# Kernel tuning notes

Measured on AMD Instinct MI355X. Metric: run time of the kernel, lower is better.

## Reference

```python
import jax, jax.numpy as jnp
import numpy as np

B, N, D, K = 32, 1024, 768, 512

def setup_inputs() -> dict:
    key = jax.random.key(0)
    k1, k2 = jax.random.split(key)
    img_feat_map = jax.random.normal(k1, (B, N, D), dtype=jnp.float32)
    codebook = jax.random.normal(k2, (K, D), dtype=jnp.float32)
    return {"img_feat_map": img_feat_map, "codebook": codebook}

def reference(img_feat_map, codebook):
    # squared L2 distances between each token and each codebook vector
    x_sq = jnp.sum(img_feat_map ** 2, axis=2, keepdims=True)          # [B,N,1]
    c_sq = jnp.sum(codebook ** 2, axis=1)[None, None, :]              # [1,1,K]
    dot = jnp.einsum('bnd,kd->bnk', img_feat_map, codebook)           # [B,N,K]
    distances = x_sq + c_sq - 2.0 * dot                               # [B,N,K]
    soft_assignments = jax.nn.softmax(-distances, axis=2)             # [B,N,K]
    # aggregate tokens per codebook slot
    aggregated = jnp.einsum('bnk,bnd->bkd', soft_assignments, img_feat_map)  # [B,K,D]
    return aggregated
```

## Files before the change

### kernel.cpp

```cpp
#include <hip/hip_runtime.h>
#include <math.h>

#define BB 32
#define NN 1024
#define DD 768
#define KK 512
#define MM (BB * NN)

typedef _Float16 half8 __attribute__((ext_vector_type(8)));
typedef _Float16 half4 __attribute__((ext_vector_type(4)));
typedef float floatx4 __attribute__((ext_vector_type(4)));

__device__ __forceinline__ void load_lds16(const void* g, void* l) {
    __builtin_amdgcn_global_load_lds(
        (const __attribute__((address_space(1))) unsigned int*)g,
        (__attribute__((address_space(3))) unsigned int*)l, 16, 0, 0);
}

__global__ __launch_bounds__(256) void prep_codebook(const float* __restrict__ cb,
                                                     _Float16* __restrict__ Cbh,
                                                     float* __restrict__ csq) {
    int k = blockIdx.x;
    const float* row = cb + (size_t)k * DD;
    _Float16* orow = Cbh + (size_t)k * DD;
    float s = 0.f;
    for (int d = threadIdx.x; d < DD; d += 256) {
        float v = row[d];
        s += v * v;
        orow[d] = (_Float16)v;
    }
    #pragma unroll
    for (int off = 32; off > 0; off >>= 1) s += __shfl_down(s, off);
    __shared__ float sm[4];
    int lane = threadIdx.x & 63, wid = threadIdx.x >> 6;
    if (lane == 0) sm[wid] = s;
    __syncthreads();
    if (threadIdx.x == 0) csq[k] = sm[0] + sm[1] + sm[2] + sm[3];
}

__global__ __launch_bounds__(512, 4) void fused_logits_softmax(
    const float* __restrict__ X,
    const _Float16* __restrict__ Cbh,
    const float* __restrict__ csq,
    _Float16* __restrict__ St,
    _Float16* __restrict__ Xt)
{
    __shared__ _Float16 Cs[2][512][32];
    __shared__ _Float16 Xs[2][64][32];
    __shared__ float redbuf[8][64];
    __shared__ float gred[64];

    const int t = threadIdx.x;
    const int w = t >> 6;
    const int lane = t & 63;
    const int l15 = lane & 15;
    const int quad = lane >> 4;
    const int wk = w * 64;
    const int gm0 = blockIdx.x * 64;
    const int b = gm0 >> 10;
    const int n0 = gm0 & 1023;

    const int qs = (quad ^ ((l15 >> 1) & 3)) * 8;

    float cs[4];
    #pragma unroll
    for (int ki = 0; ki < 4; ki++) cs[ki] = csq[wk + ki * 16 + l15];

    floatx4 acc[4][4] = {};

    const int cr = t >> 2;
    const int cq = (t & 3) ^ ((t >> 3) & 3);
    const float* xsrc = X + (size_t)(gm0 + cr) * DD + cq * 8;

    const int tdr = t >> 4;
    const int tn4 = (t & 15) * 4;

    float4 xa, xb;
    if (t < 256) { xa = *(const float4*)xsrc; xb = *(const float4*)(xsrc + 4); }

    #pragma unroll
    for (int c = 0; c < 4; c++)
        load_lds16(Cbh + (size_t)(c * 128 + cr) * DD + cq * 8,
                   (_Float16*)Cs[0] + (c * 512 + t) * 8);
    if (t < 256) {
        half8 h;
        h[0] = (_Float16)xa.x; h[1] = (_Float16)xa.y; h[2] = (_Float16)xa.z; h[3] = (_Float16)xa.w;
        h[4] = (_Float16)xb.x; h[5] = (_Float16)xb.y; h[6] = (_Float16)xb.z; h[7] = (_Float16)xb.w;
        *(half8*)&Xs[0][cr][(t & 3) * 8] = h;
        xa = *(const float4*)(xsrc + 32);
        xb = *(const float4*)(xsrc + 36);
    }
    __syncthreads();

    int cur = 0;
    for (int it = 0; it < 24; ++it) {
        const int d0 = it * 32;
        if (it + 1 < 24) {
            const int d0n = d0 + 32;
            #pragma unroll
            for (int c = 0; c < 4; c++)
                load_lds16(Cbh + (size_t)(c * 128 + cr) * DD + d0n + cq * 8,
                           (_Float16*)Cs[cur ^ 1] + (c * 512 + t) * 8);
            if (t < 256) {
                half8 h;
                h[0] = (_Float16)xa.x; h[1] = (_Float16)xa.y; h[2] = (_Float16)xa.z; h[3] = (_Float16)xa.w;
                h[4] = (_Float16)xb.x; h[5] = (_Float16)xb.y; h[6] = (_Float16)xb.z; h[7] = (_Float16)xb.w;
                *(half8*)&Xs[cur ^ 1][cr][(t & 3) * 8] = h;
                if (it + 2 < 24) {
                    xa = *(const float4*)(xsrc + (it + 2) * 32);
                    xb = *(const float4*)(xsrc + (it + 2) * 32 + 4);
                }
            }
        }
        {
            half4 xo;
            #pragma unroll
            for (int j = 0; j < 4; j++) {
                int n = tn4 + j;
                xo[j] = *((const _Float16*)Xs[cur] + n * 32 +
                          (((tdr >> 3) ^ ((n >> 1) & 3)) << 3) + (tdr & 7));
            }
            *(half4*)&Xt[((size_t)b * DD + d0 + tdr) * NN + n0 + tn4] = xo;
        }
        half8 af[4], bf[4];
        #pragma unroll
        for (int mi = 0; mi < 4; mi++)
            af[mi] = *(half8*)((_Float16*)Xs[cur] + (mi * 16 + l15) * 32 + qs);
        #pragma unroll
        for (int ki = 0; ki < 4; ki++)
            bf[ki] = *(half8*)((_Float16*)Cs[cur] + (wk + ki * 16 + l15) * 32 + qs);
        #pragma unroll
        for (int mi = 0; mi < 4; mi++)
            #pragma unroll
            for (int ki = 0; ki < 4; ki++)
                acc[mi][ki] = __builtin_amdgcn_mfma_f32_16x16x32_f16(af[mi], bf[ki], acc[mi][ki], 0, 0, 0);
        if (it + 1 < 24) { __syncthreads(); cur ^= 1; }
    }

    float pmax[4][4];
    #pragma unroll
    for (int mi = 0; mi < 4; mi++)
        #pragma unroll
        for (int r = 0; r < 4; r++) {
            float m = -1e30f;
            #pragma unroll
            for (int ki = 0; ki < 4; ki++)
                m = fmaxf(m, 2.f * acc[mi][ki][r] - cs[ki]);
            pmax[mi][r] = m;
        }
    #pragma unroll
    for (int off = 1; off < 16; off <<= 1)
        #pragma unroll
        for (int mi = 0; mi < 4; mi++)
            #pragma unroll
            for (int r = 0; r < 4; r++)
                pmax[mi][r] = fmaxf(pmax[mi][r], __shfl_xor(pmax[mi][r], off));
    if (l15 == 0) {
        #pragma unroll
        for (int mi = 0; mi < 4; mi++)
            #pragma unroll
            for (int r = 0; r < 4; r++)
                redbuf[w][mi * 16 + quad * 4 + r] = pmax[mi][r];
    }
    __syncthreads();
    if (t < 64) {
        float g = redbuf[0][t];
        #pragma unroll
        for (int wv = 1; wv < 8; wv++) g = fmaxf(g, redbuf[wv][t]);
        gred[t] = g;
    }
    __syncthreads();
    float gmax[4][4];
    #pragma unroll
    for (int mi = 0; mi < 4; mi++)
        #pragma unroll
        for (int r = 0; r < 4; r++)
            gmax[mi][r] = gred[mi * 16 + quad * 4 + r];

    float psum[4][4] = {};
    #pragma unroll
    for (int mi = 0; mi < 4; mi++)
        #pragma unroll
        for (int ki = 0; ki < 4; ki++) {
            floatx4 e;
            #pragma unroll
            for (int r = 0; r < 4; r++) {
                e[r] = __expf(2.f * acc[mi][ki][r] - cs[ki] - gmax[mi][r]);
                psum[mi][r] += e[r];
            }
            acc[mi][ki] = e;
        }
    #pragma unroll
    for (int off = 1; off < 16; off <<= 1)
        #pragma unroll
        for (int mi = 0; mi < 4; mi++)
            #pragma unroll
            for (int r = 0; r < 4; r++)
                psum[mi][r] += __shfl_xor(psum[mi][r], off);
    if (l15 == 0) {
        #pragma unroll
        for (int mi = 0; mi < 4; mi++)
            #pragma unroll
            for (int r = 0; r < 4; r++)
                redbuf[w][mi * 16 + quad * 4 + r] = psum[mi][r];
    }
    __syncthreads();
    if (t < 64) {
        float s = redbuf[0][t];
        #pragma unroll
        for (int wv = 1; wv < 8; wv++) s += redbuf[wv][t];
        gred[t] = 1.f / s;
    }
    __syncthreads();
    float ginv[4][4];
    #pragma unroll
    for (int mi = 0; mi < 4; mi++)
        #pragma unroll
        for (int r = 0; r < 4; r++)
            ginv[mi][r] = gred[mi * 16 + quad * 4 + r];

    #pragma unroll
    for (int mi = 0; mi < 4; mi++)
        #pragma unroll
        for (int ki = 0; ki < 4; ki++) {
            half4 s4;
            #pragma unroll
            for (int r = 0; r < 4; r++)
                s4[r] = (_Float16)(acc[mi][ki][r] * ginv[mi][r]);
            int k = wk + ki * 16 + l15;
            *(half4*)&St[((size_t)b * KK + k) * NN + n0 + mi * 16 + quad * 4] = s4;
        }
}

__global__ __launch_bounds__(256, 4) void gemm2_mfma(const _Float16* __restrict__ St,
                                                     const _Float16* __restrict__ Xt,
                                                     float* __restrict__ out) {
    __shared__ _Float16 As[2][128][32];
    __shared__ _Float16 Bs[2][128][32];

    const int d0 = blockIdx.x * 128;
    const int k0 = blockIdx.y * 128;
    const int b = blockIdx.z;
    const int t = threadIdx.x;
    const int wave = t >> 6;
    const int lane = t & 63;
    const int wm = (wave >> 1) * 64;
    const int wn = (wave & 1) * 64;
    const int l15 = lane & 15;
    const int quad = lane >> 4;
    const int qs = (quad ^ ((l15 >> 1) & 3)) * 8;

    const int cr = t >> 2;
    const int cq = (t & 3) ^ ((t >> 3) & 3);

    floatx4 acc[4][4] = {};

    const _Float16* Abase = St + ((size_t)b * KK + k0) * NN;
    const _Float16* Bbase = Xt + ((size_t)b * DD + d0) * NN;

    #pragma unroll
    for (int c = 0; c < 2; c++) {
        load_lds16(Abase + (size_t)(c * 64 + cr) * NN + cq * 8,
                   (_Float16*)As[0] + (c * 256 + t) * 8);
        load_lds16(Bbase + (size_t)(c * 64 + cr) * NN + cq * 8,
                   (_Float16*)Bs[0] + (c * 256 + t) * 8);
    }
    __syncthreads();

    int cur = 0;
    for (int it = 0; it < 32; ++it) {
        if (it + 1 < 32) {
            const int n0 = (it + 1) * 32;
            #pragma unroll
            for (int c = 0; c < 2; c++) {
                load_lds16(Abase + (size_t)(c * 64 + cr) * NN + n0 + cq * 8,
                           (_Float16*)As[cur ^ 1] + (c * 256 + t) * 8);
                load_lds16(Bbase + (size_t)(c * 64 + cr) * NN + n0 + cq * 8,
                           (_Float16*)Bs[cur ^ 1] + (c * 256 + t) * 8);
            }
        }
        half8 af[4], bf[4];
        #pragma unroll
        for (int i = 0; i < 4; i++) af[i] = *(half8*)&As[cur][wm + i * 16 + l15][qs];
        #pragma unroll
        for (int i = 0; i < 4; i++) bf[i] = *(half8*)&Bs[cur][wn + i * 16 + l15][qs];
        #pragma unroll
        for (int mi = 0; mi < 4; mi++)
            #pragma unroll
            for (int ni = 0; ni < 4; ni++)
                acc[mi][ni] = __builtin_amdgcn_mfma_f32_16x16x32_f16(af[mi], bf[ni], acc[mi][ni], 0, 0, 0);
        if (it + 1 < 32) { __syncthreads(); cur ^= 1; }
    }

    #pragma unroll
    for (int ni = 0; ni < 4; ni++) {
        #pragma unroll
        for (int mi = 0; mi < 4; mi++) {
            int k = k0 + wm + mi * 16 + quad * 4;
            int d = d0 + wn + ni * 16 + l15;
            float* op = out + ((size_t)b * KK + k) * DD + d;
            floatx4 a = acc[mi][ni];
            op[0 * DD] = a[0];
            op[1 * DD] = a[1];
            op[2 * DD] = a[2];
            op[3 * DD] = a[3];
        }
    }
}

extern "C" void kernel_launch(void* const* d_in, const int* in_sizes, int n_in,
                              void* d_out, int out_size, void* d_ws, size_t ws_size,
                              hipStream_t stream) {
    const float* x  = (const float*)d_in[0];
    const float* cb = (const float*)d_in[1];
    float* out = (float*)d_out;

    char* ws = (char*)d_ws;
    float*    csq = (float*)ws;
    _Float16* Cbh = (_Float16*)(ws + 4096);
    _Float16* Xt  = (_Float16*)(ws + 4096 + 786432);
    _Float16* St  = (_Float16*)(ws + 4096 + 786432 + 50331648);

    prep_codebook<<<KK, 256, 0, stream>>>(cb, Cbh, csq);

    fused_logits_softmax<<<MM / 64, 512, 0, stream>>>(x, Cbh, csq, St, Xt);

    gemm2_mfma<<<dim3(DD / 128, KK / 128, BB), 256, 0, stream>>>(St, Xt, out);
}
```

Measured before the change: 274.4 us.

## Load MFMA operands directly from global into registers, bypassing LDS staging

Both GEMM kernels stop staging the codebook, St and Xt tiles through shared memory. Each wave now loads its MFMA fragments straight from global memory into registers, double-buffered in registers. The first kernel also writes the transposed X tile from MFMA A-fragments held in registers, and it replaces __syncthreads with a barrier that waits only on lgkmcnt. The aim is to cut LDS traffic, LDS footprint and barrier cost, at the price of more redundant global/L2 reads across waves and less coalesced 16-byte strided accesses.

```diff
diff --git a/kernel.cpp b/kernel.cpp
--- a/kernel.cpp
+++ b/kernel.cpp
@@ -11,10 +11,9 @@
 typedef _Float16 half4 __attribute__((ext_vector_type(4)));
 typedef float floatx4 __attribute__((ext_vector_type(4)));
 
-__device__ __forceinline__ void load_lds16(const void* g, void* l) {
-    __builtin_amdgcn_global_load_lds(
-        (const __attribute__((address_space(1))) unsigned int*)g,
-        (__attribute__((address_space(3))) unsigned int*)l, 16, 0, 0);
+__device__ __forceinline__ void bar_lds() {
+    asm volatile("s_waitcnt lgkmcnt(0)" ::: "memory");
+    __builtin_amdgcn_s_barrier();
 }
 
 __global__ __launch_bounds__(256) void prep_codebook(const float* __restrict__ cb,
@@ -45,7 +44,6 @@
     _Float16* __restrict__ St,
     _Float16* __restrict__ Xt)
 {
-    __shared__ _Float16 Cs[2][512][32];
     __shared__ _Float16 Xs[2][64][32];
     __shared__ float redbuf[8][64];
     __shared__ float gred[64];
@@ -72,16 +70,13 @@
     const int cq = (t & 3) ^ ((t >> 3) & 3);
     const float* xsrc = X + (size_t)(gm0 + cr) * DD + cq * 8;
 
-    const int tdr = t >> 4;
-    const int tn4 = (t & 15) * 4;
+    const _Float16* cbp = Cbh + (size_t)(wk + l15) * DD + quad * 8;
+
+    _Float16* xtp = Xt + ((size_t)b * DD + quad * 8) * NN + n0 + (w & 3) * 16 + l15;
 
     float4 xa, xb;
     if (t < 256) { xa = *(const float4*)xsrc; xb = *(const float4*)(xsrc + 4); }
 
-    #pragma unroll
-    for (int c = 0; c < 4; c++)
-        load_lds16(Cbh + (size_t)(c * 128 + cr) * DD + cq * 8,
-                   (_Float16*)Cs[0] + (c * 512 + t) * 8);
     if (t < 256) {
         half8 h;
         h[0] = (_Float16)xa.x; h[1] = (_Float16)xa.y; h[2] = (_Float16)xa.z; h[3] = (_Float16)xa.w;
@@ -90,51 +85,52 @@
         xa = *(const float4*)(xsrc + 32);
         xb = *(const float4*)(xsrc + 36);
     }
-    __syncthreads();
-
-    int cur = 0;
+    half8 bfc[4], bfn[4];
+    #pragma unroll
+    for (int ki = 0; ki < 4; ki++)
+        bfc[ki] = *(const half8*)(cbp + (size_t)(ki * 16) * DD);
+    bar_lds();
+
     for (int it = 0; it < 24; ++it) {
-        const int d0 = it * 32;
-        if (it + 1 < 24) {
-            const int d0n = d0 + 32;
-            #pragma unroll
-            for (int c = 0; c < 4; c++)
-                load_lds16(Cbh + (size_t)(c * 128 + cr) * DD + d0n + cq * 8,
-                           (_Float16*)Cs[cur ^ 1] + (c * 512 + t) * 8);
+        const int cur = it & 1;
+        if (it < 23) {
             if (t < 256) {
                 half8 h;
                 h[0] = (_Float16)xa.x; h[1] = (_Float16)xa.y; h[2] = (_Float16)xa.z; h[3] = (_Float16)xa.w;
                 h[4] = (_Float16)xb.x; h[5] = (_Float16)xb.y; h[6] = (_Float16)xb.z; h[7] = (_Float16)xb.w;
                 *(half8*)&Xs[cur ^ 1][cr][(t & 3) * 8] = h;
-                if (it + 2 < 24) {
+                if (it < 22) {
                     xa = *(const float4*)(xsrc + (it + 2) * 32);
                     xb = *(const float4*)(xsrc + (it + 2) * 32 + 4);
                 }
             }
-        }
-        {
-            half4 xo;
-            #pragma unroll
-            for (int j = 0; j < 4; j++) {
-                int n = tn4 + j;
-                xo[j] = *((const _Float16*)Xs[cur] + n * 32 +
-                          (((tdr >> 3) ^ ((n >> 1) & 3)) << 3) + (tdr & 7));
-            }
-            *(half4*)&Xt[((size_t)b * DD + d0 + tdr) * NN + n0 + tn4] = xo;
-        }
-        half8 af[4], bf[4];
+            #pragma unroll
+            for (int ki = 0; ki < 4; ki++)
+                bfn[ki] = *(const half8*)(cbp + (size_t)(ki * 16) * DD + (it + 1) * 32);
+        }
+        half8 af[4];
         #pragma unroll
         for (int mi = 0; mi < 4; mi++)
             af[mi] = *(half8*)((_Float16*)Xs[cur] + (mi * 16 + l15) * 32 + qs);
         #pragma unroll
-        for (int ki = 0; ki < 4; ki++)
-            bf[ki] = *(half8*)((_Float16*)Cs[cur] + (wk + ki * 16 + l15) * 32 + qs);
-        #pragma unroll
         for (int mi = 0; mi < 4; mi++)
             #pragma unroll
             for (int ki = 0; ki < 4; ki++)
-                acc[mi][ki] = __builtin_amdgcn_mfma_f32_16x16x32_f16(af[mi], bf[ki], acc[mi][ki], 0, 0, 0);
-        if (it + 1 < 24) { __syncthreads(); cur ^= 1; }
+                acc[mi][ki] = __builtin_amdgcn_mfma_f32_16x16x32_f16(af[mi], bfc[ki], acc[mi][ki], 0, 0, 0);
+        if (w < 4) {
+            #pragma unroll
+            for (int mi = 0; mi < 4; mi++)
+                if (mi == w) {
+                    #pragma unroll
+                    for (int j = 0; j < 8; j++)
+                        xtp[(size_t)(it * 32 + j) * NN] = af[mi][j];
+                }
+        }
+        if (it < 23) {
+            bar_lds();
+            #pragma unroll
+            for (int ki = 0; ki < 4; ki++) bfc[ki] = bfn[ki];
+        }
     }
 
     float pmax[4][4];
@@ -162,20 +158,21 @@
             for (int r = 0; r < 4; r++)
                 redbuf[w][mi * 16 + quad * 4 + r] = pmax[mi][r];
     }
-    __syncthreads();
+    bar_lds();
     if (t < 64) {
         float g = redbuf[0][t];
         #pragma unroll
         for (int wv = 1; wv < 8; wv++) g = fmaxf(g, redbuf[wv][t]);
         gred[t] = g;
     }
-    __syncthreads();
+    bar_lds();
     float gmax[4][4];
     #pragma unroll
     for (int mi = 0; mi < 4; mi++)
         #pragma unroll
         for (int r = 0; r < 4; r++)
             gmax[mi][r] = gred[mi * 16 + quad * 4 + r];
+    bar_lds();
 
     float psum[4][4] = {};
     #pragma unroll
@@ -204,14 +201,14 @@
             for (int r = 0; r < 4; r++)
                 redbuf[w][mi * 16 + quad * 4 + r] = psum[mi][r];
     }
-    __syncthreads();
+    bar_lds();
     if (t < 64) {
         float s = redbuf[0][t];
         #pragma unroll
         for (int wv = 1; wv < 8; wv++) s += redbuf[wv][t];
         gred[t] = 1.f / s;
     }
-    __syncthreads();
+    bar_lds();
     float ginv[4][4];
     #pragma unroll
     for (int mi = 0; mi < 4; mi++)
@@ -235,9 +232,6 @@
 __global__ __launch_bounds__(256, 4) void gemm2_mfma(const _Float16* __restrict__ St,
                                                      const _Float16* __restrict__ Xt,
                                                      float* __restrict__ out) {
-    __shared__ _Float16 As[2][128][32];
-    __shared__ _Float16 Bs[2][128][32];
-
     const int d0 = blockIdx.x * 128;
     const int k0 = blockIdx.y * 128;
     const int b = blockIdx.z;
@@ -248,48 +242,42 @@
     const int wn = (wave & 1) * 64;
     const int l15 = lane & 15;
     const int quad = lane >> 4;
-    const int qs = (quad ^ ((l15 >> 1) & 3)) * 8;
-
-    const int cr = t >> 2;
-    const int cq = (t & 3) ^ ((t >> 3) & 3);
 
     floatx4 acc[4][4] = {};
 
-    const _Float16* Abase = St + ((size_t)b * KK + k0) * NN;
-    const _Float16* Bbase = Xt + ((size_t)b * DD + d0) * NN;
-
-    #pragma unroll
-    for (int c = 0; c < 2; c++) {
-        load_lds16(Abase + (size_t)(c * 64 + cr) * NN + cq * 8,
-                   (_Float16*)As[0] + (c * 256 + t) * 8);
-        load_lds16(Bbase + (size_t)(c * 64 + cr) * NN + cq * 8,
-                   (_Float16*)Bs[0] + (c * 256 + t) * 8);
-    }
-    __syncthreads();
-
-    int cur = 0;
-    for (int it = 0; it < 32; ++it) {
-        if (it + 1 < 32) {
-            const int n0 = (it + 1) * 32;
-            #pragma unroll
-            for (int c = 0; c < 2; c++) {
-                load_lds16(Abase + (size_t)(c * 64 + cr) * NN + n0 + cq * 8,
-                           (_Float16*)As[cur ^ 1] + (c * 256 + t) * 8);
-                load_lds16(Bbase + (size_t)(c * 64 + cr) * NN + n0 + cq * 8,
-                           (_Float16*)Bs[cur ^ 1] + (c * 256 + t) * 8);
+    const _Float16* Ab = St + ((size_t)b * KK + k0 + wm + l15) * NN + quad * 8;
+    const _Float16* Bb = Xt + ((size_t)b * DD + d0 + wn + l15) * NN + quad * 8;
+
+    half8 a0[4], b0[4], a1[4], b1[4];
+    #pragma unroll
+    for (int i = 0; i < 4; i++) {
+        a0[i] = *(const half8*)(Ab + (size_t)(i * 16) * NN);
+        b0[i] = *(const half8*)(Bb + (size_t)(i * 16) * NN);
+    }
+
+    for (int n0 = 0; n0 < NN; n0 += 64) {
+        #pragma unroll
+        for (int i = 0; i < 4; i++) {
+            a1[i] = *(const half8*)(Ab + (size_t)(i * 16) * NN + n0 + 32);
+            b1[i] = *(const half8*)(Bb + (size_t)(i * 16) * NN + n0 + 32);
+        }
+        #pragma unroll
+        for (int mi = 0; mi < 4; mi++)
+            #pragma unroll
+            for (int ni = 0; ni < 4; ni++)
+                acc[mi][ni] = __builtin_amdgcn_mfma_f32_16x16x32_f16(a0[mi], b0[ni], acc[mi][ni], 0, 0, 0);
+        if (n0 + 64 < NN) {
+            #pragma unroll
+            for (int i = 0; i < 4; i++) {
+                a0[i] = *(const half8*)(Ab + (size_t)(i * 16) * NN + n0 + 64);
+                b0[i] = *(const half8*)(Bb + (size_t)(i * 16) * NN + n0 + 64);
             }
         }
-        half8 af[4], bf[4];
-        #pragma unroll
-        for (int i = 0; i < 4; i++) af[i] = *(half8*)&As[cur][wm + i * 16 + l15][qs];
-        #pragma unroll
-        for (int i = 0; i < 4; i++) bf[i] = *(half8*)&Bs[cur][wn + i * 16 + l15][qs];
         #pragma unroll
         for (int mi = 0; mi < 4; mi++)
             #pragma unroll
             for (int ni = 0; ni < 4; ni++)
-                acc[mi][ni] = __builtin_amdgcn_mfma_f32_16x16x32_f16(af[mi], bf[ni], acc[mi][ni], 0, 0, 0);
-        if (it + 1 < 32) { __syncthreads(); cur ^= 1; }
+                acc[mi][ni] = __builtin_amdgcn_mfma_f32_16x16x32_f16(a1[mi], b1[ni], acc[mi][ni], 0, 0, 0);
     }
 
     #pragma unroll
```

Measured after the change: 397.2 us. 1.45x slower.
